# Performance work log

Measured on AMD Instinct MI355X. Metric: run time of the kernel, lower is better.

Reference implementation:

```python
import jax, jax.numpy as jnp
import numpy as np

K = 8192
D = 512
BETA = 0.25


def setup_inputs() -> dict:
    key = jax.random.key(0)
    k_z, k_cb = jax.random.split(key)
    z = jax.random.normal(k_z, (8, 4096, D), dtype=jnp.float32)
    codebook = jax.random.normal(k_cb, (K, D), dtype=jnp.float32)
    return {"z": z, "codebook": codebook}


def reference(z, codebook):
    B, Q, Din = z.shape
    flat = z.reshape(-1, Din)                      # (N, D)
    x2 = jnp.sum(flat * flat, axis=1, keepdims=True)   # (N, 1)
    e2 = jnp.sum(codebook * codebook, axis=1)          # (K,)
    xe = flat @ codebook.T                             # (N, K)
    distances = x2 - 2.0 * xe + e2[None, :]
    indices = jnp.argmin(distances, axis=1)            # (N,)
    z_q = codebook[indices].reshape(B, Q, Din)

    codebook_loss = jnp.mean((z_q - jax.lax.stop_gradient(z)) ** 2)
    commitment_loss = jnp.mean((z - jax.lax.stop_gradient(z_q)) ** 2)
    vq_loss = codebook_loss + BETA * commitment_loss
    z_q_ste = z + jax.lax.stop_gradient(z_q - z)

    # perplexity from one-hot usage counts of this batch
    N = flat.shape[0]
    counts = jnp.zeros((codebook.shape[0],), dtype=jnp.float32).at[indices].add(1.0)
    probs = counts / jnp.asarray(N, dtype=jnp.float32)
    perplexity = jnp.exp(-jnp.sum(probs * jnp.log(probs + 1e-10)))

    return z_q_ste, vq_loss, indices.reshape(B, Q), perplexity
```

## Files before the change

kernel.cpp:

```cpp
#include <hip/hip_runtime.h>
#include <hip/hip_bf16.h>

#define K_CODES 8192
#define DIM     512
#define N_VEC   32768
#define MARGIN  0.35f

typedef __attribute__((ext_vector_type(8))) short   short8;
typedef __attribute__((ext_vector_type(8))) unsigned short ushort8;
typedef __attribute__((ext_vector_type(4))) float   float4x;

__device__ inline void gl_lds16(const void* g, void* l) {
    __builtin_amdgcn_global_load_lds(
        (const __attribute__((address_space(1))) unsigned int*)g,
        (__attribute__((address_space(3))) unsigned int*)l, 16, 0, 0);
}

__device__ inline unsigned short f2bf(float f) {
    unsigned int u = __float_as_uint(f);
    return (unsigned short)((u + 0x7FFFu + ((u >> 16) & 1u)) >> 16);
}

__global__ __launch_bounds__(256) void vq_prep(
    const float* __restrict__ z, const float* __restrict__ cb,
    float* __restrict__ x2, float* __restrict__ hne2,
    unsigned short* __restrict__ zh, unsigned short* __restrict__ ch) {
    int wave = threadIdx.x >> 6;
    int lane = threadIdx.x & 63;
    int row  = blockIdx.x * 4 + wave;
    bool isZ = row < N_VEC;
    int lr = isZ ? row : row - N_VEC;
    const float* src = isZ ? z + (size_t)row * DIM : cb + (size_t)lr * DIM;

    const float4* s4 = (const float4*)src;
    float4 v0 = s4[lane * 2];
    float4 v1 = s4[lane * 2 + 1];
    float f[8] = {v0.x, v0.y, v0.z, v0.w, v1.x, v1.y, v1.z, v1.w};

    float s = 0.0f;
    ushort8 h8;
#pragma unroll
    for (int i = 0; i < 8; ++i) { s += f[i] * f[i]; h8[i] = f2bf(f[i]); }
    ((ushort8*)(isZ ? zh : ch))[(size_t)lr * 64 + lane] = h8;

#pragma unroll
    for (int off = 32; off >= 1; off >>= 1) s += __shfl_xor(s, off, 64);
    if (lane == 0) {
        if (isZ) x2[lr] = s;
        else     hne2[lr] = -0.5f * s;
    }
}

__global__ __launch_bounds__(256, 2) void vq_gemm(
    const unsigned short* __restrict__ zh, const unsigned short* __restrict__ ch,
    const float* __restrict__ hne2,
    float* __restrict__ pG, int* __restrict__ pN, float* __restrict__ pG2,
    int* __restrict__ pN2, float* __restrict__ pG3) {
    __shared__ short8 AsC[1024];
    __shared__ short8 BsC[2048];

    const int tid  = threadIdx.x;
    const int w    = tid >> 6;
    const int lane = tid & 63;
    const int wM   = w & 1;
    const int wN   = w >> 1;
    const int rowBase   = blockIdx.x * 128;
    const int half      = blockIdx.y;
    const int codeBase0 = half * 4096;

    const int low3 = lane & 7, m15 = lane & 15, hi4 = lane >> 4;

    unsigned aOff[4];
#pragma unroll
    for (int i = 0; i < 4; ++i) {
        int cell = (w * 4 + i) * 64 + lane;
        int r = cell >> 3, qs = cell & 7, q = qs ^ (r & 7);
        aOff[i] = ((unsigned)(rowBase + r) * DIM + q * 8) * 2;
    }
    unsigned bOff[8];
#pragma unroll
    for (int i = 0; i < 8; ++i) {
        int cell = (w * 8 + i) * 64 + lane;
        int c = cell >> 3, qs = cell & 7, q = qs ^ (c & 7);
        bOff[i] = ((unsigned)c * DIM + q * 8) * 2;
    }

    int rIdx[4], cIdx[8];
#pragma unroll
    for (int mf = 0; mf < 4; ++mf) rIdx[mf] = (wM * 64 + mf * 16 + m15) * 8;
#pragma unroll
    for (int nf = 0; nf < 8; ++nf) cIdx[nf] = (wN * 128 + nf * 16 + m15) * 8;

    float g1v[4][4], g2v[4][4], g3v[4][4];
    unsigned nn[4][4];
#pragma unroll
    for (int mf = 0; mf < 4; ++mf)
#pragma unroll
        for (int rg = 0; rg < 4; ++rg) {
            g1v[mf][rg] = -3.4e38f; g2v[mf][rg] = -3.4e38f;
            g3v[mf][rg] = -3.4e38f; nn[mf][rg] = 0u;
        }

    const char* pA = (const char*)zh;
    for (int ct = 0; ct < 16; ++ct) {
        const int codeBase = codeBase0 + ct * 256;
        const char* pB = (const char*)ch + (size_t)codeBase * (DIM * 2);
        float4x acc[4][8];
#pragma unroll
        for (int mf = 0; mf < 4; ++mf)
#pragma unroll
            for (int nf = 0; nf < 8; ++nf) acc[mf][nf] = (float4x){0.f, 0.f, 0.f, 0.f};

        for (int dc = 0; dc < DIM; dc += 64) {
            const int dc2 = dc * 2;
            __syncthreads();
#pragma unroll
            for (int i = 0; i < 4; ++i)
                gl_lds16(pA + aOff[i] + dc2, &AsC[(w * 4 + i) * 64]);
#pragma unroll
            for (int i = 0; i < 8; ++i)
                gl_lds16(pB + bOff[i] + dc2, &BsC[(w * 8 + i) * 64]);
            __syncthreads();

#pragma unroll
            for (int ks = 0; ks < 2; ++ks) {
                const int qx = (ks * 4 + hi4) ^ low3;
                short8 a[4];
#pragma unroll
                for (int mf = 0; mf < 4; ++mf) a[mf] = AsC[rIdx[mf] + qx];
#pragma unroll
                for (int nf = 0; nf < 8; ++nf) {
                    short8 b = BsC[cIdx[nf] + qx];
#pragma unroll
                    for (int mf = 0; mf < 4; ++mf)
                        acc[mf][nf] = __builtin_amdgcn_mfma_f32_16x16x32_bf16(
                            a[mf], b, acc[mf][nf], 0, 0, 0);
                }
            }
        }

#pragma unroll
        for (int nf = 0; nf < 8; ++nf) {
            int nb = codeBase + wN * 128 + nf * 16 + m15;
            float hv = hne2[nb];
#pragma unroll
            for (int mf = 0; mf < 4; ++mf) {
#pragma unroll
                for (int rg = 0; rg < 4; ++rg) {
                    float g = acc[mf][nf][rg] + hv;
                    bool t1 = g > g1v[mf][rg];
                    bool t2 = g > g2v[mf][rg];
                    g3v[mf][rg] = t2 ? g2v[mf][rg] : fmaxf(g3v[mf][rg], g);
                    unsigned nup = t1 ? ((nn[mf][rg] << 16) | (unsigned)nb)
                                      : (((unsigned)nb << 16) | (nn[mf][rg] & 0xFFFFu));
                    nn[mf][rg]  = t2 ? nup : nn[mf][rg];
                    g2v[mf][rg] = t1 ? g1v[mf][rg] : (t2 ? g : g2v[mf][rg]);
                    g1v[mf][rg] = t1 ? g : g1v[mf][rg];
                }
            }
        }
    }

#pragma unroll
    for (int mf = 0; mf < 4; ++mf)
#pragma unroll
        for (int rg = 0; rg < 4; ++rg) {
            float a1 = g1v[mf][rg], a2 = g2v[mf][rg], a3 = g3v[mf][rg];
            int an1 = (int)(nn[mf][rg] & 0xFFFFu);
            int an2 = (int)(nn[mf][rg] >> 16);
#pragma unroll
            for (int off = 1; off <= 8; off <<= 1) {
                float b1 = __shfl_xor(a1, off, 64);
                float b2 = __shfl_xor(a2, off, 64);
                float b3 = __shfl_xor(a3, off, 64);
                int  bn1 = __shfl_xor(an1, off, 64);
                int  bn2 = __shfl_xor(an2, off, 64);
                if (b1 > a1 || (b1 == a1 && bn1 < an1)) {
                    a3 = a2; a2 = a1; an2 = an1; a1 = b1; an1 = bn1;
                } else if (b1 > a2 || (b1 == a2 && bn1 < an2)) {
                    a3 = a2; a2 = b1; an2 = bn1;
                } else a3 = fmaxf(a3, b1);
                if (b2 > a1 || (b2 == a1 && bn2 < an1)) {
                    a3 = a2; a2 = a1; an2 = an1; a1 = b2; an1 = bn2;
                } else if (b2 > a2 || (b2 == a2 && bn2 < an2)) {
                    a3 = a2; a2 = b2; an2 = bn2;
                } else a3 = fmaxf(a3, b2);
                a3 = fmaxf(a3, b3);
            }
            if (m15 == 0) {
                int row  = rowBase + wM * 64 + mf * 16 + hi4 * 4 + rg;
                int slot = half * 2 + wN;
                pG [slot * N_VEC + row] = a1;
                pN [slot * N_VEC + row] = an1;
                pG2[slot * N_VEC + row] = a2;
                pN2[slot * N_VEC + row] = an2;
                pG3[slot * N_VEC + row] = a3;
            }
        }
}

__global__ __launch_bounds__(256) void vq_scan(
    float* __restrict__ pG, const int* __restrict__ pN,
    const float* __restrict__ pG2, const int* __restrict__ pN2,
    const float* __restrict__ pG3,
    int* __restrict__ provIdx, int* __restrict__ flags,
    unsigned long long* __restrict__ keys,
    int* __restrict__ rescueRows, int* __restrict__ rescueCnt,
    int* __restrict__ pairRows, int* __restrict__ pairCnt,
    int* __restrict__ mergedN2) {
    int r = blockIdx.x * 256 + threadIdx.x;
    float g1 = pG[r], g2 = pG2[r], g3 = pG3[r];
    int   n1 = pN[r], n2 = pN2[r];
#pragma unroll
    for (int s = 1; s < 4; ++s) {
        float a1 = pG [s * N_VEC + r];
        int  an1 = pN [s * N_VEC + r];
        float a2 = pG2[s * N_VEC + r];
        int  an2 = pN2[s * N_VEC + r];
        float a3 = pG3[s * N_VEC + r];
        if (a1 > g1 || (a1 == g1 && an1 < n1)) {
            g3 = g2; g2 = g1; n2 = n1; g1 = a1; n1 = an1;
        } else if (a1 > g2 || (a1 == g2 && an1 < n2)) {
            g3 = g2; g2 = a1; n2 = an1;
        } else g3 = fmaxf(g3, a1);
        if (a2 > g1 || (a2 == g1 && an2 < n1)) {
            g3 = g2; g2 = g1; n2 = n1; g1 = a2; n1 = an2;
        } else if (a2 > g2 || (a2 == g2 && an2 < n2)) {
            g3 = g2; g2 = a2; n2 = an2;
        } else g3 = fmaxf(g3, a2);
        g3 = fmaxf(g3, a3);
    }
    provIdx[r] = n1;
    pG[r] = g1;
    int fl = 0;
    if (g1 - g3 < MARGIN) {
        fl = 1; keys[r] = ~0ull;
        int p = atomicAdd(rescueCnt, 1);
        rescueRows[p] = r;
    } else if (g1 - g2 < MARGIN) {
        fl = 1; keys[r] = ~0ull;
        mergedN2[r] = n2;
        int p = atomicAdd(pairCnt, 1);
        pairRows[p] = r;
    }
    flags[r] = fl;
}

__global__ __launch_bounds__(256) void vq_pair(
    const float* __restrict__ z, const float* __restrict__ cb,
    const float* __restrict__ hne2,
    const int* __restrict__ provIdx, const int* __restrict__ mergedN2,
    const int* __restrict__ pairRows, const int* __restrict__ pairCnt,
    unsigned long long* __restrict__ keys) {
    const int lane = threadIdx.x & 63;
    const int wid  = blockIdx.x * 4 + (threadIdx.x >> 6);
    const int nW   = gridDim.x * 4;
    const int cnt  = *pairCnt;
    for (int i = wid; i < cnt; i += nW) {
        int r  = pairRows[i];
        int n1 = provIdx[r];
        int n2 = mergedN2[r];
        const float4* xz = (const float4*)(z  + (size_t)r  * DIM);
        const float4* c1 = (const float4*)(cb + (size_t)n1 * DIM);
        const float4* c2 = (const float4*)(cb + (size_t)n2 * DIM);
        float4 x0 = xz[lane * 2], x1 = xz[lane * 2 + 1];
        float4 a0 = c1[lane * 2], a1 = c1[lane * 2 + 1];
        float4 b0 = c2[lane * 2], b1 = c2[lane * 2 + 1];
        float d1 = x0.x*a0.x + x0.y*a0.y + x0.z*a0.z + x0.w*a0.w
                 + x1.x*a1.x + x1.y*a1.y + x1.z*a1.z + x1.w*a1.w;
        float d2 = x0.x*b0.x + x0.y*b0.y + x0.z*b0.z + x0.w*b0.w
                 + x1.x*b1.x + x1.y*b1.y + x1.z*b1.z + x1.w*b1.w;
#pragma unroll
        for (int off = 32; off >= 1; off >>= 1) {
            d1 += __shfl_xor(d1, off, 64);
            d2 += __shfl_xor(d2, off, 64);
        }
        if (lane == 0) {
            float kv1 = -hne2[n1] - d1;
            float kv2 = -hne2[n2] - d2;
            int nsel; float kv;
            if (kv2 < kv1 || (kv2 == kv1 && n2 < n1)) { kv = kv2; nsel = n2; }
            else                                      { kv = kv1; nsel = n1; }
            keys[r] = ((unsigned long long)__float_as_uint(kv) << 32) |
                      (unsigned long long)(unsigned)nsel;
        }
    }
}

#define RBM 64
#define RBK 256
#define RBD 32

__global__ __launch_bounds__(256, 2) void vq_rescue(
    const float* __restrict__ z, const float* __restrict__ cb,
    const float* __restrict__ hne2,
    const int* __restrict__ rescueRows, const int* __restrict__ rescueCnt,
    unsigned long long* __restrict__ keys) {
    __shared__ float As[RBD][RBM];
    __shared__ float Bs[RBD][RBK];
    __shared__ int   rowOf[RBM];

    const int tid = threadIdx.x;
    const int tx  = tid & 31;
    const int ty  = tid >> 5;
    const int cnt = *rescueCnt;
    const int codeBase0 = blockIdx.y * 512;
    const int sw = (tx & 8) ? 4 : 0;
    const int sRow = tid >> 2;
    const int sQ   = tid & 3;

    for (int rt = blockIdx.x; rt * RBM < cnt; rt += gridDim.x) {
        const int slotBase = rt * RBM;
        __syncthreads();
        if (tid < RBM) rowOf[tid] = rescueRows[slotBase + tid];
        __syncthreads();

        float best[8];
        int   bidx[8];
#pragma unroll
        for (int i = 0; i < 8; ++i) { best[i] = 3.4e38f; bidx[i] = K_CODES; }

        for (int kt = 0; kt < 2; ++kt) {
            const int codeBase = codeBase0 + kt * RBK;
            float acc[8][8];
#pragma unroll
            for (int i = 0; i < 8; ++i)
#pragma unroll
                for (int j = 0; j < 8; ++j) acc[i][j] = 0.0f;

            for (int dc = 0; dc < DIM; dc += RBD) {
                __syncthreads();
                {
                    const float* srcA = z + (size_t)rowOf[sRow] * DIM + dc + sQ * 8;
                    float4 va0 = ((const float4*)srcA)[0];
                    float4 va1 = ((const float4*)srcA)[1];
                    int c0 = sQ * 8;
                    As[c0 + 0][sRow] = va0.x; As[c0 + 1][sRow] = va0.y;
                    As[c0 + 2][sRow] = va0.z; As[c0 + 3][sRow] = va0.w;
                    As[c0 + 4][sRow] = va1.x; As[c0 + 5][sRow] = va1.y;
                    As[c0 + 6][sRow] = va1.z; As[c0 + 7][sRow] = va1.w;
                }
                {
                    const float4* srcB = (const float4*)(cb + (size_t)(codeBase + tid) * DIM + dc);
#pragma unroll
                    for (int j = 0; j < 8; ++j) {
                        float4 v = srcB[j];
                        Bs[j * 4 + 0][tid] = v.x; Bs[j * 4 + 1][tid] = v.y;
                        Bs[j * 4 + 2][tid] = v.z; Bs[j * 4 + 3][tid] = v.w;
                    }
                }
                __syncthreads();

#pragma unroll
                for (int d = 0; d < RBD; ++d) {
                    float a[8], b[8];
                    *(float4*)&a[0] = *(const float4*)&As[d][ty * 8];
                    *(float4*)&a[4] = *(const float4*)&As[d][ty * 8 + 4];
                    *(float4*)&b[0] = *(const float4*)&Bs[d][tx * 8 + sw];
                    *(float4*)&b[4] = *(const float4*)&Bs[d][tx * 8 + (sw ^ 4)];
#pragma unroll
                    for (int i = 0; i < 8; ++i)
#pragma unroll
                        for (int j = 0; j < 8; ++j) acc[i][j] += a[i] * b[j];
                }
            }

#pragma unroll
            for (int j = 0; j < 8; ++j) {
                int code = codeBase + tx * 8 + ((j < 4) ? (sw + j) : ((sw ^ 4) + j - 4));
                float ev = -hne2[code];
#pragma unroll
                for (int i = 0; i < 8; ++i) {
                    float kv = ev - acc[i][j];
                    if (kv < best[i] || (kv == best[i] && code < bidx[i])) {
                        best[i] = kv;
                        bidx[i] = code;
                    }
                }
            }
        }

#pragma unroll
        for (int off = 16; off >= 1; off >>= 1) {
#pragma unroll
            for (int i = 0; i < 8; ++i) {
                float od = __shfl_xor(best[i], off, 64);
                int   oi = __shfl_xor(bidx[i], off, 64);
                if (od < best[i] || (od == best[i] && oi < bidx[i])) {
                    best[i] = od;
                    bidx[i] = oi;
                }
            }
        }

        if (tx == 0) {
#pragma unroll
            for (int i = 0; i < 8; ++i) {
                int slot = slotBase + ty * 8 + i;
                if (slot < cnt) {
                    unsigned long long key =
                        ((unsigned long long)__float_as_uint(best[i]) << 32) |
                        (unsigned long long)(unsigned)bidx[i];
                    atomicMin(&keys[rowOf[ty * 8 + i]], key);
                }
            }
        }
    }
}

__global__ __launch_bounds__(256) void vq_final(
    const float* __restrict__ gBest, const int* __restrict__ provIdx,
    const int* __restrict__ flags, const unsigned long long* __restrict__ keys,
    const float* __restrict__ x2, const float* __restrict__ cb,
    float* __restrict__ zq, float* __restrict__ idxf,
    float* __restrict__ counts, float* __restrict__ lossAcc) {
    __shared__ int   sIdx[256];
    __shared__ float wsum[4];
    const int tid = threadIdx.x;
    const int r   = blockIdx.x * 256 + tid;

    int n; float dist;
    if (flags[r]) {
        unsigned long long k = keys[r];
        n = (int)(unsigned)(k & 0xffffffffu);
        float kv = __uint_as_float((unsigned)(k >> 32));
        dist = x2[r] + 2.0f * kv;
    } else {
        n = provIdx[r];
        dist = x2[r] - 2.0f * gBest[r];
    }
    sIdx[tid] = n;
    idxf[r]   = (float)n;
    atomicAdd(&counts[n], 1.0f);

    float ls = dist;
#pragma unroll
    for (int off = 32; off >= 1; off >>= 1) ls += __shfl_xor(ls, off, 64);
    if ((tid & 63) == 0) wsum[tid >> 6] = ls;
    __syncthreads();
    if (tid == 0) atomicAdd(lossAcc, wsum[0] + wsum[1] + wsum[2] + wsum[3]);

    const float4* cb4 = (const float4*)cb;
    float4* zq4 = (float4*)(zq + (size_t)blockIdx.x * 256 * DIM);
    for (int t = tid; t < 256 * (DIM / 4); t += 256) {
        int row = t >> 7, f4 = t & 127;
        zq4[(size_t)row * 128 + f4] = cb4[(size_t)sIdx[row] * 128 + f4];
    }
}

__global__ __launch_bounds__(256) void vq_finalize(const float* __restrict__ counts,
                                                   const float* __restrict__ lossAcc,
                                                   float* __restrict__ out_loss,
                                                   float* __restrict__ out_perp) {
    __shared__ float wsum[4];
    int tid = threadIdx.x;
    float s = 0.0f;
    for (int i = tid; i < K_CODES; i += 256) {
        float p = counts[i] * (1.0f / (float)N_VEC);
        s += p * logf(p + 1e-10f);
    }
#pragma unroll
    for (int off = 32; off >= 1; off >>= 1) s += __shfl_xor(s, off, 64);
    if ((tid & 63) == 0) wsum[tid >> 6] = s;
    __syncthreads();
    if (tid == 0) {
        *out_perp = expf(-(wsum[0] + wsum[1] + wsum[2] + wsum[3]));
        *out_loss = 1.25f * lossAcc[0] / (float)(N_VEC * DIM);
    }
}

extern "C" void kernel_launch(void* const* d_in, const int* in_sizes, int n_in,
                              void* d_out, int out_size, void* d_ws, size_t ws_size,
                              hipStream_t stream) {
    (void)in_sizes; (void)n_in; (void)out_size; (void)ws_size;
    const float* z  = (const float*)d_in[0];
    const float* cb = (const float*)d_in[1];

    char* ws = (char*)d_ws;
    float* x2        = (float*)(ws + 0);
    float* hne2      = (float*)(ws + 131072);
    float* counts    = (float*)(ws + 163840);
    float* lossAcc   = (float*)(ws + 196608);
    int*   rescueCnt = (int*)  (ws + 196612);
    int*   pairCnt   = (int*)  (ws + 196616);
    int*   provIdx   = (int*)  (ws + 262144);
    int*   flags     = (int*)  (ws + 393216);
    unsigned long long* keys = (unsigned long long*)(ws + 524288);
    int*   rescueRows = (int*) (ws + 786432);
    float* pG        = (float*)(ws + 1048576);
    int*   pN        = (int*)  (ws + 1572864);
    float* pG2       = (float*)(ws + 2097152);
    unsigned short* zh = (unsigned short*)(ws + 2621440);
    unsigned short* ch = (unsigned short*)(ws + 36175872);

    float* out      = (float*)d_out;
    float* zq       = out;
    float* out_loss = out + 16777216;
    float* idxf     = out + 16777217;
    float* out_perp = out + 16777217 + 32768;

    char* sc = (char*)d_out;
    int*   pN2      = (int*)  (sc + 0);
    float* pG3      = (float*)(sc + 524288);
    int*   mergedN2 = (int*)  (sc + 1048576);
    int*   pairRows = (int*)  (sc + 1179648);

    hipMemsetAsync(counts, 0, 32768 + 16, stream);
    hipMemsetAsync(rescueRows, 0, 131072, stream);
    vq_prep<<<(N_VEC + K_CODES) / 4, 256, 0, stream>>>(z, cb, x2, hne2, zh, ch);
    dim3 grid(N_VEC / 128, 2);
    vq_gemm<<<grid, 256, 0, stream>>>(zh, ch, hne2, pG, pN, pG2, pN2, pG3);
    vq_scan<<<N_VEC / 256, 256, 0, stream>>>(pG, pN, pG2, pN2, pG3, provIdx, flags,
                                             keys, rescueRows, rescueCnt,
                                             pairRows, pairCnt, mergedN2);
    vq_pair<<<128, 256, 0, stream>>>(z, cb, hne2, provIdx, mergedN2,
                                     pairRows, pairCnt, keys);
    dim3 rgrid(64, 16);
    vq_rescue<<<rgrid, 256, 0, stream>>>(z, cb, hne2, rescueRows, rescueCnt, keys);
    vq_final<<<N_VEC / 256, 256, 0, stream>>>(pG, provIdx, flags, keys, x2, cb,
                                              zq, idxf, counts, lossAcc);
    vq_finalize<<<1, 256, 0, stream>>>(counts, lossAcc, out_loss, out_perp);
}
```

Baseline: 738.3 us.

## Pack code tags into score low bits and track top-3 with med3

The GEMM epilogue now stores an 11-bit code tag in the low mantissa bits of each score. Top-3 tracking becomes branch-free fmed3/fmax operations, which replaces the separate index bookkeeping and the compare-heavy shuffle merge. Because truncating those bits makes scores less precise, MARGIN is raised to keep exact rescue correct, which can send more rows to rescue. The rescue kernel is also reshaped to one 256-code tile per block with a strided B-fragment access and a 32x32 grid.

```diff
diff --git a/kernel.cpp b/kernel.cpp
--- a/kernel.cpp
+++ b/kernel.cpp
@@ -4,7 +4,7 @@
 #define K_CODES 8192
 #define DIM     512
 #define N_VEC   32768
-#define MARGIN  0.35f
+#define MARGIN  0.5f
 
 typedef __attribute__((ext_vector_type(8))) short   short8;
 typedef __attribute__((ext_vector_type(8))) unsigned short ushort8;
@@ -19,6 +19,10 @@
 __device__ inline unsigned short f2bf(float f) {
     unsigned int u = __float_as_uint(f);
     return (unsigned short)((u + 0x7FFFu + ((u >> 16) & 1u)) >> 16);
+}
+
+__device__ inline float med3(float a, float b, float c) {
+    return __builtin_amdgcn_fmed3f(a, b, c);
 }
 
 __global__ __launch_bounds__(256) void vq_prep(
@@ -92,13 +96,11 @@
     for (int nf = 0; nf < 8; ++nf) cIdx[nf] = (wN * 128 + nf * 16 + m15) * 8;
 
     float g1v[4][4], g2v[4][4], g3v[4][4];
-    unsigned nn[4][4];
 #pragma unroll
     for (int mf = 0; mf < 4; ++mf)
 #pragma unroll
         for (int rg = 0; rg < 4; ++rg) {
-            g1v[mf][rg] = -3.4e38f; g2v[mf][rg] = -3.4e38f;
-            g3v[mf][rg] = -3.4e38f; nn[mf][rg] = 0u;
+            g1v[mf][rg] = -3.4e38f; g2v[mf][rg] = -3.4e38f; g3v[mf][rg] = -3.4e38f;
         }
 
     const char* pA = (const char*)zh;
@@ -143,19 +145,17 @@
         for (int nf = 0; nf < 8; ++nf) {
             int nb = codeBase + wN * 128 + nf * 16 + m15;
             float hv = hne2[nb];
+            unsigned tag = ((unsigned)ct << 7) | ((unsigned)nf << 4) | (unsigned)m15;
 #pragma unroll
             for (int mf = 0; mf < 4; ++mf) {
 #pragma unroll
                 for (int rg = 0; rg < 4; ++rg) {
-                    float g = acc[mf][nf][rg] + hv;
-                    bool t1 = g > g1v[mf][rg];
-                    bool t2 = g > g2v[mf][rg];
-                    g3v[mf][rg] = t2 ? g2v[mf][rg] : fmaxf(g3v[mf][rg], g);
-                    unsigned nup = t1 ? ((nn[mf][rg] << 16) | (unsigned)nb)
-                                      : (((unsigned)nb << 16) | (nn[mf][rg] & 0xFFFFu));
-                    nn[mf][rg]  = t2 ? nup : nn[mf][rg];
-                    g2v[mf][rg] = t1 ? g1v[mf][rg] : (t2 ? g : g2v[mf][rg]);
-                    g1v[mf][rg] = t1 ? g : g1v[mf][rg];
+                    float g  = acc[mf][nf][rg] + hv;
+                    float pk = __uint_as_float(
+                        (__float_as_uint(g) & 0xFFFFF800u) | tag);
+                    g3v[mf][rg] = med3(pk, g2v[mf][rg], g3v[mf][rg]);
+                    g2v[mf][rg] = med3(pk, g1v[mf][rg], g2v[mf][rg]);
+                    g1v[mf][rg] = fmaxf(g1v[mf][rg], pk);
                 }
             }
         }
@@ -166,35 +166,32 @@
 #pragma unroll
         for (int rg = 0; rg < 4; ++rg) {
             float a1 = g1v[mf][rg], a2 = g2v[mf][rg], a3 = g3v[mf][rg];
-            int an1 = (int)(nn[mf][rg] & 0xFFFFu);
-            int an2 = (int)(nn[mf][rg] >> 16);
 #pragma unroll
             for (int off = 1; off <= 8; off <<= 1) {
                 float b1 = __shfl_xor(a1, off, 64);
                 float b2 = __shfl_xor(a2, off, 64);
                 float b3 = __shfl_xor(a3, off, 64);
-                int  bn1 = __shfl_xor(an1, off, 64);
-                int  bn2 = __shfl_xor(an2, off, 64);
-                if (b1 > a1 || (b1 == a1 && bn1 < an1)) {
-                    a3 = a2; a2 = a1; an2 = an1; a1 = b1; an1 = bn1;
-                } else if (b1 > a2 || (b1 == a2 && bn1 < an2)) {
-                    a3 = a2; a2 = b1; an2 = bn1;
-                } else a3 = fmaxf(a3, b1);
-                if (b2 > a1 || (b2 == a1 && bn2 < an1)) {
-                    a3 = a2; a2 = a1; an2 = an1; a1 = b2; an1 = bn2;
-                } else if (b2 > a2 || (b2 == a2 && bn2 < an2)) {
-                    a3 = a2; a2 = b2; an2 = bn2;
-                } else a3 = fmaxf(a3, b2);
-                a3 = fmaxf(a3, b3);
+                a3 = med3(b1, a2, a3);
+                a2 = med3(b1, a1, a2);
+                a1 = fmaxf(a1, b1);
+                a3 = med3(b2, a2, a3);
+                a2 = med3(b2, a1, a2);
+                a3 = med3(b3, a2, a3);
             }
             if (m15 == 0) {
+                unsigned u1 = __float_as_uint(a1);
+                unsigned u2 = __float_as_uint(a2);
+                unsigned u3 = __float_as_uint(a3);
+                int t1 = (int)(u1 & 0x7FFu), t2 = (int)(u2 & 0x7FFu);
+                int c1 = codeBase0 + ((t1 & 0x780) << 1) + wN * 128 + (t1 & 0x7F);
+                int c2 = codeBase0 + ((t2 & 0x780) << 1) + wN * 128 + (t2 & 0x7F);
                 int row  = rowBase + wM * 64 + mf * 16 + hi4 * 4 + rg;
                 int slot = half * 2 + wN;
-                pG [slot * N_VEC + row] = a1;
-                pN [slot * N_VEC + row] = an1;
-                pG2[slot * N_VEC + row] = a2;
-                pN2[slot * N_VEC + row] = an2;
-                pG3[slot * N_VEC + row] = a3;
+                pG [slot * N_VEC + row] = __uint_as_float(u1 & 0xFFFFF800u);
+                pN [slot * N_VEC + row] = c1;
+                pG2[slot * N_VEC + row] = __uint_as_float(u2 & 0xFFFFF800u);
+                pN2[slot * N_VEC + row] = c2;
+                pG3[slot * N_VEC + row] = __uint_as_float(u3 & 0xFFFFF800u);
             }
         }
 }
@@ -304,8 +301,7 @@
     const int tx  = tid & 31;
     const int ty  = tid >> 5;
     const int cnt = *rescueCnt;
-    const int codeBase0 = blockIdx.y * 512;
-    const int sw = (tx & 8) ? 4 : 0;
+    const int codeBase = blockIdx.y * RBK;
     const int sRow = tid >> 2;
     const int sQ   = tid & 3;
 
@@ -315,67 +311,64 @@
         if (tid < RBM) rowOf[tid] = rescueRows[slotBase + tid];
         __syncthreads();
 
+        float acc[8][8];
+#pragma unroll
+        for (int i = 0; i < 8; ++i)
+#pragma unroll
+            for (int j = 0; j < 8; ++j) acc[i][j] = 0.0f;
+
+        for (int dc = 0; dc < DIM; dc += RBD) {
+            __syncthreads();
+            {
+                const float* srcA = z + (size_t)rowOf[sRow] * DIM + dc + sQ * 8;
+                float4 va0 = ((const float4*)srcA)[0];
+                float4 va1 = ((const float4*)srcA)[1];
+                int c0 = sQ * 8;
+                As[c0 + 0][sRow] = va0.x; As[c0 + 1][sRow] = va0.y;
+                As[c0 + 2][sRow] = va0.z; As[c0 + 3][sRow] = va0.w;
+                As[c0 + 4][sRow] = va1.x; As[c0 + 5][sRow] = va1.y;
+                As[c0 + 6][sRow] = va1.z; As[c0 + 7][sRow] = va1.w;
+            }
+            {
+                const float4* srcB = (const float4*)(cb + (size_t)(codeBase + tid) * DIM + dc);
+#pragma unroll
+                for (int j = 0; j < 8; ++j) {
+                    float4 v = srcB[j];
+                    Bs[j * 4 + 0][tid] = v.x; Bs[j * 4 + 1][tid] = v.y;
+                    Bs[j * 4 + 2][tid] = v.z; Bs[j * 4 + 3][tid] = v.w;
+                }
+            }
+            __syncthreads();
+
+#pragma unroll
+            for (int d = 0; d < RBD; ++d) {
+                float a[8], b[8];
+                *(float4*)&a[0] = *(const float4*)&As[d][ty * 8];
+                *(float4*)&a[4] = *(const float4*)&As[d][ty * 8 + 4];
+#pragma unroll
+                for (int j = 0; j < 8; ++j) b[j] = Bs[d][tx + 32 * j];
+#pragma unroll
+                for (int i = 0; i < 8; ++i)
+#pragma unroll
+                    for (int j = 0; j < 8; ++j) acc[i][j] += a[i] * b[j];
+            }
+        }
+
         float best[8];
         int   bidx[8];
 #pragma unroll
         for (int i = 0; i < 8; ++i) { best[i] = 3.4e38f; bidx[i] = K_CODES; }
 
-        for (int kt = 0; kt < 2; ++kt) {
-            const int codeBase = codeBase0 + kt * RBK;
-            float acc[8][8];
-#pragma unroll
-            for (int i = 0; i < 8; ++i)
-#pragma unroll
-                for (int j = 0; j < 8; ++j) acc[i][j] = 0.0f;
-
-            for (int dc = 0; dc < DIM; dc += RBD) {
-                __syncthreads();
-                {
-                    const float* srcA = z + (size_t)rowOf[sRow] * DIM + dc + sQ * 8;
-                    float4 va0 = ((const float4*)srcA)[0];
-                    float4 va1 = ((const float4*)srcA)[1];
-                    int c0 = sQ * 8;
-                    As[c0 + 0][sRow] = va0.x; As[c0 + 1][sRow] = va0.y;
-                    As[c0 + 2][sRow] = va0.z; As[c0 + 3][sRow] = va0.w;
-                    As[c0 + 4][sRow] = va1.x; As[c0 + 5][sRow] = va1.y;
-                    As[c0 + 6][sRow] = va1.z; As[c0 + 7][sRow] = va1.w;
-                }
-                {
-                    const float4* srcB = (const float4*)(cb + (size_t)(codeBase + tid) * DIM + dc);
-#pragma unroll
-                    for (int j = 0; j < 8; ++j) {
-                        float4 v = srcB[j];
-                        Bs[j * 4 + 0][tid] = v.x; Bs[j * 4 + 1][tid] = v.y;
-                        Bs[j * 4 + 2][tid] = v.z; Bs[j * 4 + 3][tid] = v.w;
-                    }
-                }
-                __syncthreads();
-
-#pragma unroll
-                for (int d = 0; d < RBD; ++d) {
-                    float a[8], b[8];
-                    *(float4*)&a[0] = *(const float4*)&As[d][ty * 8];
-                    *(float4*)&a[4] = *(const float4*)&As[d][ty * 8 + 4];
-                    *(float4*)&b[0] = *(const float4*)&Bs[d][tx * 8 + sw];
-                    *(float4*)&b[4] = *(const float4*)&Bs[d][tx * 8 + (sw ^ 4)];
-#pragma unroll
-                    for (int i = 0; i < 8; ++i)
-#pragma unroll
-                        for (int j = 0; j < 8; ++j) acc[i][j] += a[i] * b[j];
-                }
-            }
-
-#pragma unroll
-            for (int j = 0; j < 8; ++j) {
-                int code = codeBase + tx * 8 + ((j < 4) ? (sw + j) : ((sw ^ 4) + j - 4));
-                float ev = -hne2[code];
-#pragma unroll
-                for (int i = 0; i < 8; ++i) {
-                    float kv = ev - acc[i][j];
-                    if (kv < best[i] || (kv == best[i] && code < bidx[i])) {
-                        best[i] = kv;
-                        bidx[i] = code;
-                    }
+#pragma unroll
+        for (int j = 0; j < 8; ++j) {
+            int code = codeBase + tx + 32 * j;
+            float ev = -hne2[code];
+#pragma unroll
+            for (int i = 0; i < 8; ++i) {
+                float kv = ev - acc[i][j];
+                if (kv < best[i] || (kv == best[i] && code < bidx[i])) {
+                    best[i] = kv;
+                    bidx[i] = code;
                 }
             }
         }
@@ -515,7 +508,7 @@
                                              pairRows, pairCnt, mergedN2);
     vq_pair<<<128, 256, 0, stream>>>(z, cb, hne2, provIdx, mergedN2,
                                      pairRows, pairCnt, keys);
-    dim3 rgrid(64, 16);
+    dim3 rgrid(32, 32);
     vq_rescue<<<rgrid, 256, 0, stream>>>(z, cb, hne2, rescueRows, rescueCnt, keys);
     vq_final<<<N_VEC / 256, 256, 0, stream>>>(pG, provIdx, flags, keys, x2, cb,
                                               zq, idxf, counts, lossAcc);
```

After: 716.4 us. 1.03x faster.
